# Optimization experiments

Hardware: AMD Instinct MI355X
Metric: run time of the kernel (lower is better)

The kernel has to match this reference:

```python
import jax, jax.numpy as jnp
import numpy as np

N_NODES = 100000
N_EDGES = 1600000
D_FEAT = 128
D_HID = 128
N_CLASSES = 10
N_GRAPHS = 128


def setup_inputs() -> dict:
    key = jax.random.key(0)
    ks = jax.random.split(key, 12)
    x = jax.random.normal(ks[0], (N_NODES, D_FEAT), dtype=jnp.float32)
    edge_index = jax.random.randint(ks[1], (2, N_EDGES), 0, N_NODES, dtype=jnp.int64)
    batch = jnp.sort(jax.random.randint(ks[2], (N_NODES,), 0, N_GRAPHS, dtype=jnp.int64))
    s = 0.05
    W0 = jax.random.normal(ks[3], (D_FEAT, D_HID), dtype=jnp.float32) * s
    b0 = jnp.zeros((D_HID,), dtype=jnp.float32)
    W1 = jax.random.normal(ks[4], (D_HID, D_HID), dtype=jnp.float32) * s
    b1 = jnp.zeros((D_HID,), dtype=jnp.float32)
    W2 = jax.random.normal(ks[5], (D_HID, D_HID), dtype=jnp.float32) * s
    b2 = jnp.zeros((D_HID,), dtype=jnp.float32)
    lin_W = jax.random.normal(ks[6], (D_HID, N_CLASSES), dtype=jnp.float32) * s
    lin_b = jnp.zeros((N_CLASSES,), dtype=jnp.float32)
    return {"x": x, "edge_index": edge_index, "batch": batch,
            "W0": W0, "b0": b0, "W1": W1, "b1": b1, "W2": W2, "b2": b2,
            "lin_W": lin_W, "lin_b": lin_b}


def gcn_layer(x, W, b, src, dst, n_nodes):
    # GCNConv: out = D^{-1/2}(A+I)D^{-1/2} (x W) + b, self-loop weight 1
    h = x @ W  # [N, D_out]
    ones = jnp.ones(src.shape[0], dtype=x.dtype)
    deg = jax.ops.segment_sum(ones, dst, num_segments=n_nodes) + 1.0  # +1 self-loop
    dinv = jax.lax.rsqrt(deg)
    norm = dinv[src] * dinv[dst]  # [E]
    agg = jax.ops.segment_sum(h[src] * norm[:, None], dst, num_segments=n_nodes)
    agg = agg + (dinv * dinv)[:, None] * h  # self-loop term: norm_ii = deg_i^{-1}
    return agg + b


def reference(x, edge_index, batch, W0, b0, W1, b1, W2, b2, lin_W, lin_b):
    n = x.shape[0]
    src, dst = edge_index[0], edge_index[1]
    x = gcn_layer(x, W0, b0, src, dst, n)
    x = jax.nn.relu(x)
    x = gcn_layer(x, W1, b1, src, dst, n)
    x = jax.nn.relu(x)
    x = gcn_layer(x, W2, b2, src, dst, n)  # no activation after last conv
    # global mean pool over graphs
    sums = jax.ops.segment_sum(x, batch, num_segments=N_GRAPHS)
    counts = jax.ops.segment_sum(jnp.ones((n,), x.dtype), batch, num_segments=N_GRAPHS)
    pooled = sums / jnp.maximum(counts, 1.0)[:, None]
    # dropout is identity in eval mode
    logits = pooled @ lin_W + lin_b
    return jax.nn.softmax(logits, axis=1)
```

## Files before the change

kernel.cpp:

```cpp
#include <hip/hip_runtime.h>
#include <hip/hip_bf16.h>

#define N_NODES  100000
#define N_EDGES  1600000
#define D_FEAT   128
#define N_GRAPHS 128
#define N_CLS    10
#define CAP      64
#define ZROW     100000

#define NB       391
#define CAPB     4608
#define CHUNK    4000
#define PCHUNK   128
#define AGG_WAVES 8192
#define WPAD     136

typedef __bf16 bf16x8 __attribute__((ext_vector_type(8)));
typedef float  f32x4  __attribute__((ext_vector_type(4)));
typedef float  f32x2  __attribute__((ext_vector_type(2)));

__global__ __launch_bounds__(256) void prepW(const float* __restrict__ W0,
                                             const float* __restrict__ W1,
                                             const float* __restrict__ W2,
                                             __bf16* __restrict__ wt,
                                             unsigned char* __restrict__ Hs) {
    int idx = blockIdx.x * 256 + threadIdx.x;
    if (blockIdx.x == 0 && threadIdx.x < 32)
        ((unsigned int*)(Hs + (size_t)ZROW * 128))[threadIdx.x] = 0u;
    if (idx >= 3 * 16384) return;
    int which = idx >> 14, e = idx & 16383;
    int k = e >> 7, n = e & 127;
    const float* W = (which == 0) ? W0 : ((which == 1) ? W1 : W2);
    wt[which * 16384 + n * 128 + k] = (__bf16)W[k * 128 + n];
}

__global__ __launch_bounds__(512) void binsort(const int* __restrict__ ei,
                                               int* __restrict__ gcur,
                                               int* __restrict__ staging) {
    __shared__ int hist[512];
    __shared__ int hscan[512];
    __shared__ int cur[512];
    __shared__ int gofs[512];
    __shared__ uint2 lbuf[CHUNK];
    int t = threadIdx.x;
    int base = blockIdx.x * CHUNK;

    hist[t] = 0;
    __syncthreads();
    for (int i = t; i < CHUNK; i += 512)
        atomicAdd(&hist[ei[N_EDGES + base + i] >> 8], 1);
    __syncthreads();
    hscan[t] = hist[t];
    __syncthreads();
    for (int off = 1; off < 512; off <<= 1) {
        int v = (t >= off) ? hscan[t - off] : 0;
        __syncthreads();
        hscan[t] += v;
        __syncthreads();
    }
    int ex = hscan[t] - hist[t];
    cur[t] = ex;
    if (t < NB && hist[t] > 0) {
        int gb = atomicAdd(&gcur[t], hist[t]);
        gofs[t] = t * CAPB + gb - ex;
    }
    __syncthreads();
    for (int i = t; i < CHUNK; i += 512) {
        unsigned src = (unsigned)ei[base + i];
        unsigned dst = (unsigned)ei[N_EDGES + base + i];
        int p = atomicAdd(&cur[dst >> 8], 1);
        lbuf[p] = make_uint2(src, dst);
    }
    __syncthreads();
    for (int i = t; i < CHUNK; i += 512) {
        uint2 v = lbuf[i];
        int b = (int)(v.y >> 8);
        staging[gofs[b] + i] = (int)(((v.y & 255u) << 24) | v.x);
    }
}

__global__ __launch_bounds__(256) void build_csr(const int* __restrict__ gcur,
                                                 const int* __restrict__ staging,
                                                 int* __restrict__ srclist,
                                                 int* __restrict__ cnt,
                                                 float* __restrict__ dinv) {
    __shared__ int slots[256 * CAP];
    __shared__ int lcnt[256];
    int t = threadIdx.x, b = blockIdx.x;
    lcnt[t] = 1;
    slots[t * CAP] = b * 256 + t;
    __syncthreads();
    int cb = gcur[b];
    if (cb > CAPB) cb = CAPB;
    const int* st = staging + b * CAPB;
    for (int i = t; i < cb; i += 256) {
        int v = st[i];
        int ld = ((unsigned)v) >> 24;
        int s = v & 0xFFFFFF;
        int p = atomicAdd(&lcnt[ld], 1);
        if (p < CAP) slots[ld * CAP + p] = s;
    }
    __syncthreads();
    int4* d4 = (int4*)(srclist + (size_t)b * 256 * CAP);
    const int4* s4 = (const int4*)slots;
    for (int j = t; j < 256 * CAP / 4; j += 256) d4[j] = s4[j];
    int node = b * 256 + t;
    if (node < N_NODES) {
        int c = lcnt[t];
        if (c > CAP) c = CAP;
        cnt[node] = c;
        dinv[node] = rsqrtf((float)c);
    }
}

template <bool A_IS_F32>
__global__ __launch_bounds__(256) void gemm128(const void* __restrict__ Ap,
                                               const __bf16* __restrict__ Wt,
                                               const float* __restrict__ dinv,
                                               unsigned char* __restrict__ Hs) {
    __shared__ __bf16 wlds[128 * WPAD];
    int t = threadIdx.x;
    int wid = (blockIdx.x * 256 + t) >> 6;
    int lane = t & 63;
    int m = lane & 15, q = lane >> 4;
    int rowbase = wid * 16;
    bool active = wid < N_NODES / 16;

    {
        const bf16x8* src = (const bf16x8*)Wt;
        for (int j = t; j < 2048; j += 256) {
            int r = j >> 4, c = (j & 15) * 8;
            *(bf16x8*)(wlds + r * WPAD + c) = src[j];
        }
    }

    bf16x8 afrag[4];
    float dv = 0.f;
    if (active) {
        dv = dinv[rowbase + m];
        if (A_IS_F32) {
            const float* A = (const float*)Ap + (size_t)(rowbase + m) * 128 + q * 8;
            f32x4 v[8];
#pragma unroll
            for (int ks = 0; ks < 4; ++ks) {
                v[2 * ks]     = *(const f32x4*)(A + ks * 32);
                v[2 * ks + 1] = *(const f32x4*)(A + ks * 32 + 4);
            }
#pragma unroll
            for (int ks = 0; ks < 4; ++ks)
#pragma unroll
                for (int j = 0; j < 4; ++j) {
                    afrag[ks][j]     = (__bf16)v[2 * ks][j];
                    afrag[ks][4 + j] = (__bf16)v[2 * ks + 1][j];
                }
        } else {
            const __bf16* A = (const __bf16*)Ap + (size_t)(rowbase + m) * 128 + q * 8;
#pragma unroll
            for (int ks = 0; ks < 4; ++ks)
                afrag[ks] = *(const bf16x8*)(A + ks * 32);
        }
    }
    __syncthreads();
    if (!active) return;

    f32x4 acc[8] = {};
#pragma unroll
    for (int ks = 0; ks < 4; ++ks) {
#pragma unroll
        for (int tj = 0; tj < 8; ++tj) {
            bf16x8 b = *(const bf16x8*)(wlds + (tj * 16 + m) * WPAD + ks * 32 + q * 8);
            acc[tj] = __builtin_amdgcn_mfma_f32_16x16x32_bf16(b, afrag[ks], acc[tj], 0, 0, 0);
        }
    }

    unsigned char* rowp = Hs + (size_t)(rowbase + m) * 128 + q * 4;
#pragma unroll
    for (int tj = 0; tj < 8; ++tj) {
        int lo = __builtin_amdgcn_cvt_pk_fp8_f32(acc[tj][0] * dv, acc[tj][1] * dv, 0, false);
        int w  = __builtin_amdgcn_cvt_pk_fp8_f32(acc[tj][2] * dv, acc[tj][3] * dv, lo, true);
        *(unsigned int*)(rowp + tj * 16) = (unsigned int)w;
    }
}

template <bool RELU>
__global__ __launch_bounds__(256, 8) void aggregate(const unsigned char* __restrict__ Hs,
                                                    const float* __restrict__ bias,
                                                    const float* __restrict__ dinv,
                                                    const int* __restrict__ cnt,
                                                    const int* __restrict__ srclist,
                                                    __bf16* __restrict__ X) {
    int wid = (blockIdx.x * 256 + threadIdx.x) >> 6;
    int lane = threadIdx.x & 63;
    int g = lane >> 4;
    int idx = lane & 15;
    unsigned rowoff = (unsigned)idx * 8;

    f32x4 bb0 = *(const f32x4*)(bias + idx * 8);
    f32x4 bb1 = *(const f32x4*)(bias + idx * 8 + 4);

    for (int node = wid; node < N_NODES; node += AGG_WAVES) {
        float di = dinv[node];
        int deg = cnt[node];
        int myS = srclist[(size_t)node * CAP + lane];

        f32x2 acc[4] = {};

        auto fetch = [&](int e) -> uint2 {
            int en = e + g;
            int se = __shfl(myS, en);
            se = (en < deg) ? se : ZROW;
            unsigned off = ((unsigned)se << 7) + rowoff;
            return *(const uint2*)(Hs + off);
        };

        uint2 v0 = fetch(0);
        uint2 v1 = fetch(4);
        uint2 v2 = fetch(8);
        for (int e = 0; e < deg; e += 4) {
            uint2 vn = fetch(e + 12);
            acc[0] += __builtin_amdgcn_cvt_pk_f32_fp8(v0.x, false);
            acc[1] += __builtin_amdgcn_cvt_pk_f32_fp8(v0.x, true);
            acc[2] += __builtin_amdgcn_cvt_pk_f32_fp8(v0.y, false);
            acc[3] += __builtin_amdgcn_cvt_pk_f32_fp8(v0.y, true);
            v0 = v1; v1 = v2; v2 = vn;
        }

        float a[8];
#pragma unroll
        for (int j = 0; j < 4; ++j) { a[2 * j] = acc[j][0]; a[2 * j + 1] = acc[j][1]; }
#pragma unroll
        for (int j = 0; j < 8; ++j) {
            a[j] += __shfl_xor(a[j], 16);
            a[j] += __shfl_xor(a[j], 32);
        }

        bf16x8 o;
#pragma unroll
        for (int j = 0; j < 8; ++j) {
            float bj = (j < 4) ? bb0[j] : bb1[j - 4];
            float t = di * a[j] + bj;
            if (RELU) t = fmaxf(t, 0.f);
            o[j] = (__bf16)t;
        }
        if (g == 0) *(bf16x8*)(X + (size_t)node * 128 + idx * 8) = o;
    }
}

__global__ __launch_bounds__(256) void pool_partial(const __bf16* __restrict__ X,
                                                    const int* __restrict__ batch,
                                                    float* __restrict__ sums) {
    int t = threadIdx.x;
    int d = t & 127, half = t >> 7;
    int start = blockIdx.x * PCHUNK;
    int end = start + PCHUNK;
    if (end > N_NODES) end = N_NODES;
    float acc = 0.f;
    int curg = -1;
    for (int i = start + half; i < end; i += 2) {
        int g = batch[i];
        if (g != curg) {
            if (curg >= 0) atomicAdd(&sums[curg * 128 + d], acc);
            acc = 0.f;
            curg = g;
        }
        acc += (float)X[(size_t)i * 128 + d];
    }
    if (curg >= 0) atomicAdd(&sums[curg * 128 + d], acc);
}

__global__ __launch_bounds__(64) void pool_final(const float* __restrict__ sums,
                                                 const int* __restrict__ batch,
                                                 const float* __restrict__ linW,
                                                 const float* __restrict__ linb,
                                                 float* __restrict__ out) {
    int g = blockIdx.x, lane = threadIdx.x;
    int bnd[2];
#pragma unroll
    for (int k = 0; k < 2; ++k) {
        int target = g + k;
        int lo = 0, hi = N_NODES;
        while (lo < hi) {
            int mid = (lo + hi) >> 1;
            if (batch[mid] < target) lo = mid + 1; else hi = mid;
        }
        bnd[k] = lo;
    }
    float c = fmaxf((float)(bnd[1] - bnd[0]), 1.f);
    float p0 = sums[g * 128 + lane] / c;
    float p1 = sums[g * 128 + 64 + lane] / c;

    float lg[N_CLS];
#pragma unroll
    for (int cc = 0; cc < N_CLS; ++cc) {
        float v = p0 * linW[lane * N_CLS + cc] + p1 * linW[(lane + 64) * N_CLS + cc];
#pragma unroll
        for (int off = 1; off < 64; off <<= 1) v += __shfl_xor(v, off);
        lg[cc] = v + linb[cc];
    }
    float mx = -1e30f;
#pragma unroll
    for (int cc = 0; cc < N_CLS; ++cc) mx = fmaxf(mx, lg[cc]);
    float ssum = 0.f;
#pragma unroll
    for (int cc = 0; cc < N_CLS; ++cc) { lg[cc] = __expf(lg[cc] - mx); ssum += lg[cc]; }
    if (lane < N_CLS) out[g * N_CLS + lane] = lg[lane] / ssum;
}

extern "C" void kernel_launch(void* const* d_in, const int* in_sizes, int n_in,
                              void* d_out, int out_size, void* d_ws, size_t ws_size,
                              hipStream_t stream) {
    const float* x     = (const float*)d_in[0];
    const int*   ei    = (const int*)d_in[1];
    const int*   batch = (const int*)d_in[2];
    const float* W0    = (const float*)d_in[3];
    const float* b0    = (const float*)d_in[4];
    const float* W1    = (const float*)d_in[5];
    const float* b1    = (const float*)d_in[6];
    const float* W2    = (const float*)d_in[7];
    const float* b2    = (const float*)d_in[8];
    const float* linW  = (const float*)d_in[9];
    const float* linb  = (const float*)d_in[10];

    char* ws = (char*)d_ws;
    int*    gcur    = (int*)(ws + 0);
    float*  sums    = (float*)(ws + 2048);
    float*  dinv    = (float*)(ws + 67584);
    int*    cnt     = (int*)(ws + 467584);
    __bf16* wt      = (__bf16*)(ws + 867584);
    int*    srclist = (int*)(ws + 965888);
    unsigned char* Hs = (unsigned char*)(ws + 26590464);
    int*    staging = (int*)(ws + 26590464);
    __bf16* xbuf    = (__bf16*)(ws + 52190464);

    hipMemsetAsync(ws, 0, 67584, stream);

    prepW<<<192, 256, 0, stream>>>(W0, W1, W2, wt, Hs);
    binsort<<<N_EDGES / CHUNK, 512, 0, stream>>>(ei, gcur, staging);
    build_csr<<<NB, 256, 0, stream>>>(gcur, staging, srclist, cnt, dinv);

    gemm128<true><<<1563, 256, 0, stream>>>(x, wt, dinv, Hs);
    aggregate<true><<<AGG_WAVES / 4, 256, 0, stream>>>(Hs, b0, dinv, cnt, srclist, xbuf);
    gemm128<false><<<1563, 256, 0, stream>>>(xbuf, wt + 16384, dinv, Hs);
    aggregate<true><<<AGG_WAVES / 4, 256, 0, stream>>>(Hs, b1, dinv, cnt, srclist, xbuf);
    gemm128<false><<<1563, 256, 0, stream>>>(xbuf, wt + 32768, dinv, Hs);
    aggregate<false><<<AGG_WAVES / 4, 256, 0, stream>>>(Hs, b2, dinv, cnt, srclist, xbuf);

    pool_partial<<<(N_NODES + PCHUNK - 1) / PCHUNK, 256, 0, stream>>>(xbuf, batch, sums);
    pool_final<<<N_GRAPHS, 64, 0, stream>>>(sums, batch, linW, linb, (float*)d_out);
}
```

Baseline: 332.3 us.

## Make GEMM persistent with register prefetch and pad CSR slots with zero-row index

The per-layer GEMM becomes a persistent kernel with a fixed grid of 1024 blocks. Each wave loops over 16-row tiles and prefetches the next tile's A rows into registers while the MFMAs for the current tile run, which spreads the LDS weight load over more work and hides global load latency. Separately, build_csr now fills every unused neighbor slot with the zero-row index. That lets the aggregate fetch drop its per-edge bounds check and select, at the cost of extra LDS initialization and a sync in build_csr.

Measured after the change: 447.4 us. 34.7% more time.

```diff
diff --git a/kernel.cpp b/kernel.cpp
--- a/kernel.cpp
+++ b/kernel.cpp
@@ -15,6 +15,8 @@
 #define PCHUNK   128
 #define AGG_WAVES 8192
 #define WPAD     136
+#define GEMM_BLOCKS 1024
+#define NTILES   6250
 
 typedef __bf16 bf16x8 __attribute__((ext_vector_type(8)));
 typedef float  f32x4  __attribute__((ext_vector_type(4)));
@@ -88,7 +90,10 @@
     __shared__ int slots[256 * CAP];
     __shared__ int lcnt[256];
     int t = threadIdx.x, b = blockIdx.x;
+    int4 z4 = make_int4(ZROW, ZROW, ZROW, ZROW);
+    for (int j = t; j < 256 * CAP / 4; j += 256) ((int4*)slots)[j] = z4;
     lcnt[t] = 1;
+    __syncthreads();
     slots[t * CAP] = b * 256 + t;
     __syncthreads();
     int cb = gcur[b];
@@ -115,18 +120,12 @@
 }
 
 template <bool A_IS_F32>
-__global__ __launch_bounds__(256) void gemm128(const void* __restrict__ Ap,
-                                               const __bf16* __restrict__ Wt,
-                                               const float* __restrict__ dinv,
-                                               unsigned char* __restrict__ Hs) {
+__global__ __launch_bounds__(256, 4) void gemm128(const void* __restrict__ Ap,
+                                                  const __bf16* __restrict__ Wt,
+                                                  const float* __restrict__ dinv,
+                                                  unsigned char* __restrict__ Hs) {
     __shared__ __bf16 wlds[128 * WPAD];
     int t = threadIdx.x;
-    int wid = (blockIdx.x * 256 + t) >> 6;
-    int lane = t & 63;
-    int m = lane & 15, q = lane >> 4;
-    int rowbase = wid * 16;
-    bool active = wid < N_NODES / 16;
-
     {
         const bf16x8* src = (const bf16x8*)Wt;
         for (int j = t; j < 2048; j += 256) {
@@ -134,52 +133,82 @@
             *(bf16x8*)(wlds + r * WPAD + c) = src[j];
         }
     }
-
-    bf16x8 afrag[4];
-    float dv = 0.f;
-    if (active) {
-        dv = dinv[rowbase + m];
+    int lane = t & 63;
+    int m = lane & 15, q = lane >> 4;
+    int wslot = (blockIdx.x << 2) + (t >> 6);
+    const int NW = GEMM_BLOCKS * 4;
+
+    f32x4 rf[8];
+    bf16x8 rb[4];
+
+    int tile = wslot;
+    if (tile < NTILES) {
+        int row = tile * 16 + m;
         if (A_IS_F32) {
-            const float* A = (const float*)Ap + (size_t)(rowbase + m) * 128 + q * 8;
-            f32x4 v[8];
+            const float* A = (const float*)Ap + (size_t)row * 128 + q * 8;
 #pragma unroll
             for (int ks = 0; ks < 4; ++ks) {
-                v[2 * ks]     = *(const f32x4*)(A + ks * 32);
-                v[2 * ks + 1] = *(const f32x4*)(A + ks * 32 + 4);
+                rf[2 * ks]     = *(const f32x4*)(A + ks * 32);
+                rf[2 * ks + 1] = *(const f32x4*)(A + ks * 32 + 4);
             }
+        } else {
+            const __bf16* A = (const __bf16*)Ap + (size_t)row * 128 + q * 8;
+#pragma unroll
+            for (int ks = 0; ks < 4; ++ks) rb[ks] = *(const bf16x8*)(A + ks * 32);
+        }
+    }
+    __syncthreads();
+
+    for (; tile < NTILES; tile += NW) {
+        bf16x8 af[4];
+        if (A_IS_F32) {
 #pragma unroll
             for (int ks = 0; ks < 4; ++ks)
 #pragma unroll
                 for (int j = 0; j < 4; ++j) {
-                    afrag[ks][j]     = (__bf16)v[2 * ks][j];
-                    afrag[ks][4 + j] = (__bf16)v[2 * ks + 1][j];
+                    af[ks][j]     = (__bf16)rf[2 * ks][j];
+                    af[ks][4 + j] = (__bf16)rf[2 * ks + 1][j];
                 }
         } else {
-            const __bf16* A = (const __bf16*)Ap + (size_t)(rowbase + m) * 128 + q * 8;
-#pragma unroll
-            for (int ks = 0; ks < 4; ++ks)
-                afrag[ks] = *(const bf16x8*)(A + ks * 32);
-        }
-    }
-    __syncthreads();
-    if (!active) return;
-
-    f32x4 acc[8] = {};
-#pragma unroll
-    for (int ks = 0; ks < 4; ++ks) {
+#pragma unroll
+            for (int ks = 0; ks < 4; ++ks) af[ks] = rb[ks];
+        }
+        float dv = dinv[tile * 16 + m];
+
+        int ntile = tile + NW;
+        if (ntile < NTILES) {
+            int nrow = ntile * 16 + m;
+            if (A_IS_F32) {
+                const float* A = (const float*)Ap + (size_t)nrow * 128 + q * 8;
+#pragma unroll
+                for (int ks = 0; ks < 4; ++ks) {
+                    rf[2 * ks]     = *(const f32x4*)(A + ks * 32);
+                    rf[2 * ks + 1] = *(const f32x4*)(A + ks * 32 + 4);
+                }
+            } else {
+                const __bf16* A = (const __bf16*)Ap + (size_t)nrow * 128 + q * 8;
+#pragma unroll
+                for (int ks = 0; ks < 4; ++ks) rb[ks] = *(const bf16x8*)(A + ks * 32);
+            }
+        }
+
+        f32x4 acc[8] = {};
+#pragma unroll
+        for (int ks = 0; ks < 4; ++ks) {
+#pragma unroll
+            for (int tj = 0; tj < 8; ++tj) {
+                bf16x8 b = *(const bf16x8*)(wlds + (tj * 16 + m) * WPAD + ks * 32 + q * 8);
+                acc[tj] = __builtin_amdgcn_mfma_f32_16x16x32_bf16(b, af[ks], acc[tj], 0, 0, 0);
+            }
+        }
+
+        unsigned char* rowp = Hs + (size_t)(tile * 16 + m) * 128 + q * 4;
 #pragma unroll
         for (int tj = 0; tj < 8; ++tj) {
-            bf16x8 b = *(const bf16x8*)(wlds + (tj * 16 + m) * WPAD + ks * 32 + q * 8);
-            acc[tj] = __builtin_amdgcn_mfma_f32_16x16x32_bf16(b, afrag[ks], acc[tj], 0, 0, 0);
-        }
-    }
-
-    unsigned char* rowp = Hs + (size_t)(rowbase + m) * 128 + q * 4;
-#pragma unroll
-    for (int tj = 0; tj < 8; ++tj) {
-        int lo = __builtin_amdgcn_cvt_pk_fp8_f32(acc[tj][0] * dv, acc[tj][1] * dv, 0, false);
-        int w  = __builtin_amdgcn_cvt_pk_fp8_f32(acc[tj][2] * dv, acc[tj][3] * dv, lo, true);
-        *(unsigned int*)(rowp + tj * 16) = (unsigned int)w;
+            int lo = __builtin_amdgcn_cvt_pk_fp8_f32(acc[tj][0] * dv, acc[tj][1] * dv, 0, false);
+            int w  = __builtin_amdgcn_cvt_pk_fp8_f32(acc[tj][2] * dv, acc[tj][3] * dv, lo, true);
+            *(unsigned int*)(rowp + tj * 16) = (unsigned int)w;
+        }
     }
 }
 
@@ -207,9 +236,7 @@
         f32x2 acc[4] = {};
 
         auto fetch = [&](int e) -> uint2 {
-            int en = e + g;
-            int se = __shfl(myS, en);
-            se = (en < deg) ? se : ZROW;
+            int se = __shfl(myS, (e + g) & 63);
             unsigned off = ((unsigned)se << 7) + rowoff;
             return *(const uint2*)(Hs + off);
         };
@@ -339,11 +366,11 @@
     binsort<<<N_EDGES / CHUNK, 512, 0, stream>>>(ei, gcur, staging);
     build_csr<<<NB, 256, 0, stream>>>(gcur, staging, srclist, cnt, dinv);
 
-    gemm128<true><<<1563, 256, 0, stream>>>(x, wt, dinv, Hs);
+    gemm128<true><<<GEMM_BLOCKS, 256, 0, stream>>>(x, wt, dinv, Hs);
     aggregate<true><<<AGG_WAVES / 4, 256, 0, stream>>>(Hs, b0, dinv, cnt, srclist, xbuf);
-    gemm128<false><<<1563, 256, 0, stream>>>(xbuf, wt + 16384, dinv, Hs);
+    gemm128<false><<<GEMM_BLOCKS, 256, 0, stream>>>(xbuf, wt + 16384, dinv, Hs);
     aggregate<true><<<AGG_WAVES / 4, 256, 0, stream>>>(Hs, b1, dinv, cnt, srclist, xbuf);
-    gemm128<false><<<1563, 256, 0, stream>>>(xbuf, wt + 32768, dinv, Hs);
+    gemm128<false><<<GEMM_BLOCKS, 256, 0, stream>>>(xbuf, wt + 32768, dinv, Hs);
     aggregate<false><<<AGG_WAVES / 4, 256, 0, stream>>>(Hs, b2, dinv, cnt, srclist, xbuf);
 
     pool_partial<<<(N_NODES + PCHUNK - 1) / PCHUNK, 256, 0, stream>>>(xbuf, batch, sums);
```
